# Performance work log

Measured on AMD Instinct MI355X. Metric: run time of the kernel, lower is better.

## Reference

```python
import jax, jax.numpy as jnp
import numpy as np

C = 256

def setup_inputs() -> dict:
    key = jax.random.key(0)
    ks = jax.random.split(key, 7)
    s = 1.0 / np.sqrt(C)
    x = jax.random.normal(ks[0], (4, C, 64, 64), dtype=jnp.float32)
    Wq = jax.random.uniform(ks[1], (C, C), jnp.float32, -s, s)
    bq = jax.random.uniform(ks[2], (C,), jnp.float32, -s, s)
    Wk = jax.random.uniform(ks[3], (C, C), jnp.float32, -s, s)
    bk = jax.random.uniform(ks[4], (C,), jnp.float32, -s, s)
    Wv = jax.random.uniform(ks[5], (C, C), jnp.float32, -s, s)
    bv = jax.random.uniform(ks[6], (C,), jnp.float32, -s, s)
    return {"x": x, "Wq": Wq, "bq": bq, "Wk": Wk, "bk": bk, "Wv": Wv, "bv": bv}

def reference(x, Wq, bq, Wk, bk, Wv, bv):
    B, Cc, H, W = x.shape
    N = H * W
    xf = x.reshape(B, Cc, N)                      # (B, C, N)
    # 1x1 conv == channel linear: out[b,o,n] = sum_c W[o,c] x[b,c,n] + b[o]
    q = jnp.einsum('oc,bcn->bno', Wq, xf) + bq    # (B, N, C)  proj_query^T
    k = jnp.einsum('oc,bcn->bon', Wk, xf) + bk[None, :, None]  # (B, C, N)
    v = jnp.einsum('oc,bcn->bon', Wv, xf) + bv[None, :, None]  # (B, C, N)
    energy = jnp.einsum('bnc,bcm->bnm', q, k)     # (B, N, N)
    attention = jax.nn.softmax(energy, axis=-1)
    # out = V @ attention^T : out[b,c,n] = sum_m v[b,c,m] * attention[b,n,m]
    out = jnp.einsum('bcm,bnm->bcn', v, attention)
    return out.reshape(B, Cc, H, W)
```

## Files before the change

kernel.cpp:

```cpp
#include <hip/hip_runtime.h>
#include <math.h>

#define BB 4
#define CC 256
#define NN 4096
#define KV 32

using half8 = __attribute__((ext_vector_type(8))) _Float16;
using f32x4 = __attribute__((ext_vector_type(4))) float;

__device__ __forceinline__ unsigned short f2h(float f) {
  _Float16 h = (_Float16)f;
  return __builtin_bit_cast(unsigned short, h);
}
__device__ __forceinline__ float h2f(unsigned short u) {
  return (float)__builtin_bit_cast(_Float16, u);
}

#define ASYNC16(g, l)                                                        \
  __builtin_amdgcn_global_load_lds(                                          \
      (const __attribute__((address_space(1))) unsigned int*)(g),            \
      (__attribute__((address_space(3))) unsigned int*)(l), 16, 0, 0)

__device__ __forceinline__ int row512_off(int r, int chunk) {
  return r * 256 + (((chunk & 24) | ((chunk ^ r) & 7)) << 3);
}
__device__ __forceinline__ int tile32_off(int r, int q) {
  return (r >> 1) * 64 + (((((r & 1) << 2) | q) ^ ((r >> 1) & 7)) & 7) * 8;
}
__device__ __forceinline__ int vt_off(int r, int chunk) {
  return r * 64 + (((chunk ^ r) & 7) << 3);
}

__global__ __launch_bounds__(256) void k_wcast(const float* __restrict__ Wq,
    const float* __restrict__ Wk, const float* __restrict__ Wv,
    unsigned short* __restrict__ Wt) {
  int id = blockIdx.x * 256 + threadIdx.x;
  int pos8 = id & 7, o = (id >> 3) & 255, ks = (id >> 11) & 3, p3 = id >> 13;
  const float* W = p3 == 0 ? Wq : (p3 == 1 ? Wk : Wv);
  int c = ks * 64 + ((pos8 ^ o) & 7) * 8;
  const float* src = W + (size_t)o * CC + c;
  float4 a = *(const float4*)(src);
  float4 b4 = *(const float4*)(src + 4);
  union { unsigned short u[8]; uint4 v4; } pk;
  pk.u[0] = f2h(a.x);  pk.u[1] = f2h(a.y);  pk.u[2] = f2h(a.z);  pk.u[3] = f2h(a.w);
  pk.u[4] = f2h(b4.x); pk.u[5] = f2h(b4.y); pk.u[6] = f2h(b4.z); pk.u[7] = f2h(b4.w);
  *(uint4*)(Wt + (size_t)id * 8) = pk.v4;
}

__global__ __launch_bounds__(512) void k_proj(const float* __restrict__ x,
    const unsigned short* __restrict__ Wt,
    const float* __restrict__ bq, const float* __restrict__ bk,
    const float* __restrict__ bv,
    unsigned short* __restrict__ Q, unsigned short* __restrict__ K,
    unsigned short* __restrict__ V) {
  __shared__ __align__(16) char ps[110848];
  float* xf = (float*)ps;
  unsigned short* xa = (unsigned short*)(ps + 8448);
  unsigned short* wh = (unsigned short*)(ps + 12544);
  int b = blockIdx.y, n0 = blockIdx.x * 32;
  int t = threadIdx.x, w = t >> 6, lane = t & 63, l15 = lane & 15, quad = lane >> 4;

  f32x4 z = {0.f, 0.f, 0.f, 0.f};
  f32x4 acc[3][2][2];
#pragma unroll
  for (int p3 = 0; p3 < 3; ++p3)
#pragma unroll
    for (int ct = 0; ct < 2; ++ct)
#pragma unroll
      for (int mt = 0; mt < 2; ++mt) acc[p3][ct][mt] = z;

  for (int ks = 0; ks < 4; ++ks) {
    if (ks) __syncthreads();
#pragma unroll
    for (int p3 = 0; p3 < 3; ++p3) {
      const char* wb = (const char*)(Wt + (size_t)(p3 * 4 + ks) * 16384);
#pragma unroll
      for (int p = 0; p < 4; ++p) {
        int c = p * 512 + t;
        ASYNC16(wb + c * 16, &wh[p3 * 16384 + (p * 512 + (w << 6)) * 8]);
      }
    }
    {
      int c = t >> 3, nl = (t & 7) * 4;
      float4 v = *(const float4*)(x + ((size_t)b * CC + ks * 64 + c) * NN + n0 + nl);
      float* d = xf + c * 33 + nl;
      d[0] = v.x; d[1] = v.y; d[2] = v.z; d[3] = v.w;
    }
    __syncthreads();
    {
      int n = t >> 4, cb = (t & 15) * 4;
      union { unsigned short u[4]; ushort4 v4; } tmp;
#pragma unroll
      for (int i = 0; i < 4; ++i) tmp.u[i] = f2h(xf[(cb + i) * 33 + n]);
      int ch = cb >> 3;
      *(ushort4*)&xa[n * 64 + (((ch ^ n) & 7) << 3) + (cb & 7)] = tmp.v4;
    }
    __syncthreads();
#pragma unroll
    for (int kc = 0; kc < 2; ++kc) {
      half8 af[2];
#pragma unroll
      for (int mt = 0; mt < 2; ++mt)
        af[mt] = *(const half8*)&xa[vt_off(mt * 16 + l15, kc * 4 + quad)];
#pragma unroll
      for (int p3 = 0; p3 < 3; ++p3)
#pragma unroll
        for (int ct = 0; ct < 2; ++ct) {
          half8 bf = *(const half8*)&wh[p3 * 16384 + vt_off(w * 32 + ct * 16 + l15, kc * 4 + quad)];
#pragma unroll
          for (int mt = 0; mt < 2; ++mt)
            acc[p3][ct][mt] = __builtin_amdgcn_mfma_f32_16x16x32_f16(af[mt], bf, acc[p3][ct][mt], 0, 0, 0);
        }
    }
  }
#pragma unroll
  for (int p3 = 0; p3 < 3; ++p3) {
    const float* bias = p3 == 0 ? bq : (p3 == 1 ? bk : bv);
#pragma unroll
    for (int ct = 0; ct < 2; ++ct) {
      float bv_ = bias[w * 32 + ct * 16 + l15];
#pragma unroll
      for (int mt = 0; mt < 2; ++mt)
#pragma unroll
        for (int r = 0; r < 4; ++r) acc[p3][ct][mt][r] += bv_;
    }
  }
#pragma unroll
  for (int p3 = 0; p3 < 2; ++p3) {
    __syncthreads();
    unsigned short* qo = (unsigned short*)ps;
#pragma unroll
    for (int ct = 0; ct < 2; ++ct)
#pragma unroll
      for (int mt = 0; mt < 2; ++mt)
#pragma unroll
        for (int r = 0; r < 4; ++r)
          qo[(mt * 16 + quad * 4 + r) * 264 + w * 32 + ct * 16 + l15] = f2h(acc[p3][ct][mt][r]);
    __syncthreads();
    unsigned short* outp = (p3 == 0 ? Q : K) + ((size_t)b * NN + n0) * CC;
#pragma unroll
    for (int p = 0; p < 2; ++p) {
      int f = p * 8192 + t * 16;
      int n = f >> 9, off = f & 511;
      *(uint4*)((char*)outp + (size_t)n * 512 + off) =
        *(const uint4*)((const char*)&qo[n * 264] + off);
    }
  }
  {
    __syncthreads();
    unsigned short* vo = (unsigned short*)ps;
#pragma unroll
    for (int ct = 0; ct < 2; ++ct)
#pragma unroll
      for (int mt = 0; mt < 2; ++mt)
#pragma unroll
        for (int r = 0; r < 4; ++r)
          vo[(w * 32 + ct * 16 + l15) * 36 + mt * 16 + quad * 4 + r] = f2h(acc[2][ct][mt][r]);
    __syncthreads();
#pragma unroll
    for (int p = 0; p < 2; ++p) {
      int id = p * 512 + t;
      int o = id >> 2, off = (id & 3) * 16;
      *(uint4*)((char*)(V + ((size_t)b * CC + o) * NN + n0) + off) =
        *(const uint4*)((const char*)&vo[o * 36] + off);
    }
  }
}

__global__ __launch_bounds__(512) void k_flash(const unsigned short* __restrict__ Q,
    const unsigned short* __restrict__ K, const unsigned short* __restrict__ V,
    float* __restrict__ out, unsigned short* __restrict__ opart,
    float* __restrict__ ml, int n_splits) {
  __shared__ __align__(16) char sm[83456];
  unsigned short* kt0 = (unsigned short*)sm;
  unsigned short* kt1 = (unsigned short*)(sm + 16384);
  unsigned short* vt0 = (unsigned short*)(sm + 32768);
  unsigned short* vt1 = (unsigned short*)(sm + 49152);
  unsigned short* pt0 = (unsigned short*)(sm + 65536);
  unsigned short* pt1 = (unsigned short*)(sm + 73728);
  float* al0 = (float*)(sm + 81920);
  float* al1 = (float*)(sm + 82432);
  float* ll  = (float*)(sm + 82944);
  int b = blockIdx.y, q0 = blockIdx.x * 128, split = blockIdx.z;
  int nt = (NN / KV) / n_splits;
  int t = threadIdx.x, w = t >> 6, lane = t & 63, l15 = lane & 15, quad = lane >> 4;
  int g = w >> 1, h = w & 1;

  half8 qf[8];
  const unsigned short* qrow = Q + ((size_t)b * NN + q0 + w * 16 + l15) * CC;
#pragma unroll
  for (int k = 0; k < 8; ++k) qf[k] = *(const half8*)(qrow + k * 32 + quad * 8);

  f32x4 z = {0.f, 0.f, 0.f, 0.f};
  f32x4 o_acc[2][8];
#pragma unroll
  for (int mt = 0; mt < 2; ++mt)
#pragma unroll
    for (int i = 0; i < 8; ++i) o_acc[mt][i] = z;
  float m_i[4], lp_[4];
#pragma unroll
  for (int r = 0; r < 4; ++r) { m_i[r] = -INFINITY; lp_[r] = 0.f; }

  int it_beg = split * nt, it_end = it_beg + nt;

  auto dma_k = [&](int it, unsigned short* dst) {
    const char* kb = (const char*)(K + ((size_t)b * NN + it * KV) * CC);
#pragma unroll
    for (int p = 0; p < 2; ++p) {
      int c = p * 512 + t;
      int r = c >> 5, lo = c & 31;
      int ch = (lo & 24) | ((lo ^ r) & 7);
      ASYNC16(kb + r * 512 + ch * 16, &dst[(p * 512 + (w << 6)) * 8]);
    }
  };
  auto dma_v = [&](int it, unsigned short* dst) {
    const char* vb = (const char*)(V + (size_t)b * CC * NN + it * KV);
#pragma unroll
    for (int p = 0; p < 2; ++p) {
      int id = p * 512 + t;
      int unit = id >> 3, u = id & 7;
      int x2 = u ^ (unit & 7);
      int r = unit * 2 + (x2 >> 2), ch = x2 & 3;
      ASYNC16(vb + (size_t)r * (NN * 2) + ch * 16, &dst[(p * 512 + (w << 6)) * 8]);
    }
  };

  auto pv_step = [&](const unsigned short* pprev, const unsigned short* vprev,
                     const float* alp) {
    f32x4 aa[2];
    aa[0] = *(const f32x4*)&alp[g * 32 + quad * 4];
    aa[1] = *(const f32x4*)&alp[g * 32 + 16 + quad * 4];
    int need = 0;
#pragma unroll
    for (int mt = 0; mt < 2; ++mt)
#pragma unroll
      for (int r = 0; r < 4; ++r) need |= (aa[mt][r] != 1.f);
    if (__any(need)) {
#pragma unroll
      for (int mt = 0; mt < 2; ++mt)
#pragma unroll
        for (int ct = 0; ct < 8; ++ct)
#pragma unroll
          for (int r = 0; r < 4; ++r) o_acc[mt][ct][r] *= aa[mt][r];
    }
    half8 af[2];
#pragma unroll
    for (int mt = 0; mt < 2; ++mt)
      af[mt] = *(const half8*)&pprev[tile32_off(g * 32 + mt * 16 + l15, quad)];
    __builtin_amdgcn_s_setprio(1);
#pragma unroll
    for (int ct = 0; ct < 8; ++ct) {
      half8 bf = *(const half8*)&vprev[tile32_off(h * 128 + ct * 16 + l15, quad)];
#pragma unroll
      for (int mt = 0; mt < 2; ++mt)
        o_acc[mt][ct] = __builtin_amdgcn_mfma_f32_16x16x32_f16(af[mt], bf, o_acc[mt][ct], 0, 0, 0);
    }
    __builtin_amdgcn_s_setprio(0);
  };

  dma_k(it_beg, (it_beg & 1) ? kt1 : kt0);

  for (int it = it_beg; it < it_end; ++it) {
    int par = it & 1;
    const unsigned short* kcur = par ? kt1 : kt0;
    unsigned short* knxt       = par ? kt0 : kt1;
    unsigned short* vcur       = par ? vt1 : vt0;
    const unsigned short* vprev = par ? vt0 : vt1;
    unsigned short* pcur       = par ? pt1 : pt0;
    const unsigned short* pprev = par ? pt0 : pt1;
    float* alc       = par ? al1 : al0;
    const float* alp = par ? al0 : al1;

    __syncthreads();

    if (it + 1 < it_end) dma_k(it + 1, knxt);
    dma_v(it, vcur);

    f32x4 sa[2];
    sa[0] = z; sa[1] = z;
    __builtin_amdgcn_s_setprio(1);
#pragma unroll
    for (int kk = 0; kk < 8; ++kk)
#pragma unroll
      for (int j = 0; j < 2; ++j) {
        half8 bf = *(const half8*)&kcur[row512_off(j * 16 + l15, kk * 4 + quad)];
        sa[j] = __builtin_amdgcn_mfma_f32_16x16x32_f16(qf[kk], bf, sa[j], 0, 0, 0);
      }
    __builtin_amdgcn_s_setprio(0);

    float mt4[4];
#pragma unroll
    for (int r = 0; r < 4; ++r) mt4[r] = fmaxf(sa[0][r], sa[1][r]);
#pragma unroll
    for (int off = 1; off < 16; off <<= 1)
#pragma unroll
      for (int r = 0; r < 4; ++r)
        mt4[r] = fmaxf(mt4[r], __shfl_xor(mt4[r], off, 64));
    float alpha[4];
#pragma unroll
    for (int r = 0; r < 4; ++r) {
      float mn = fmaxf(m_i[r], mt4[r]);
      alpha[r] = __expf(m_i[r] - mn);
      m_i[r] = mn;
    }
#pragma unroll
    for (int r = 0; r < 4; ++r) {
      float ls = 0.f;
#pragma unroll
      for (int j = 0; j < 2; ++j) {
        float p = __expf(sa[j][r] - m_i[r]);
        sa[j][r] = p;
        ls += p;
      }
      lp_[r] = lp_[r] * alpha[r] + ls;
    }
    if (l15 == 0) {
      f32x4 a4 = {alpha[0], alpha[1], alpha[2], alpha[3]};
      *(f32x4*)&alc[w * 16 + quad * 4] = a4;
    }
#pragma unroll
    for (int j = 0; j < 2; ++j)
#pragma unroll
      for (int r = 0; r < 4; ++r) {
        int row = w * 16 + quad * 4 + r;
        int ch = 2 * j + (l15 >> 3);
        pcur[tile32_off(row, ch) + (l15 & 7)] = f2h(sa[j][r]);
      }

    if (it > it_beg) pv_step(pprev, vprev, alp);
  }

  {
    int par = (it_end - 1) & 1;
    __syncthreads();
    pv_step(par ? pt1 : pt0, par ? vt1 : vt0, par ? al1 : al0);
  }

#pragma unroll
  for (int off = 1; off < 16; off <<= 1)
#pragma unroll
    for (int r = 0; r < 4; ++r)
      lp_[r] += __shfl_xor(lp_[r], off, 64);
  if (l15 == 0) {
#pragma unroll
    for (int r = 0; r < 4; ++r) ll[w * 16 + quad * 4 + r] = lp_[r];
  }
  if (n_splits != 1 && l15 == 0) {
    size_t qi = (size_t)q0 + w * 16 + quad * 4;
    float* mp = ml + ((size_t)(split * 2 + 0) * BB + b) * NN + qi;
    float* lq = ml + ((size_t)(split * 2 + 1) * BB + b) * NN + qi;
#pragma unroll
    for (int r = 0; r < 4; ++r) { mp[r] = m_i[r]; lq[r] = lp_[r]; }
  }
  __syncthreads();
  float sc[2][4];
#pragma unroll
  for (int mt = 0; mt < 2; ++mt)
#pragma unroll
    for (int r = 0; r < 4; ++r) {
      float lv = ll[g * 32 + mt * 16 + quad * 4 + r];
      sc[mt][r] = (n_splits == 1) ? 1.f / lv : 1.f;
    }

  float* od = (float*)sm;
  float* obf = out + (size_t)b * CC * NN + q0;
  unsigned short* obh = opart + ((size_t)split * BB + b) * CC * NN + q0;
#pragma unroll
  for (int pp = 0; pp < 8; ++pp) {
    __syncthreads();
    if (h == (pp >> 2)) {
#pragma unroll
      for (int cp = 0; cp < 2; ++cp) {
        int ct = (pp & 3) * 2 + cp;
#pragma unroll
        for (int mt = 0; mt < 2; ++mt)
#pragma unroll
          for (int r = 0; r < 4; ++r)
            od[(cp * 16 + l15) * 132 + g * 32 + mt * 16 + quad * 4 + r] =
                o_acc[mt][ct][r] * sc[mt][r];
      }
    }
    __syncthreads();
    if (n_splits == 1) {
#pragma unroll
      for (int p2 = 0; p2 < 2; ++p2) {
        int row = p2 * 16 + (t >> 5);
        *(float4*)(obf + (size_t)(pp * 32 + row) * NN + (t & 31) * 4) =
          *(const float4*)&od[row * 132 + (t & 31) * 4];
      }
    } else {
      int row = t >> 4, q8 = (t & 15) * 8;
      union { unsigned short u[8]; uint4 v4; } tmp;
#pragma unroll
      for (int i2 = 0; i2 < 8; ++i2) tmp.u[i2] = f2h(od[row * 132 + q8 + i2]);
      *(uint4*)(obh + (size_t)(pp * 32 + row) * NN + q8) = tmp.v4;
    }
  }
}

__global__ __launch_bounds__(256) void k_merge(const unsigned short* __restrict__ opart,
    const float* __restrict__ ml, float* __restrict__ out) {
  size_t i = ((size_t)blockIdx.x * 256 + threadIdx.x) * 4;
  int n = (int)(i & (NN - 1));
  int b = (int)(i >> 20);
  float4 m1 = *(const float4*)(ml + ((size_t)(0 * BB) + b) * NN + n);
  float4 l1 = *(const float4*)(ml + ((size_t)(1 * BB) + b) * NN + n);
  float4 m2 = *(const float4*)(ml + ((size_t)(2 * BB) + b) * NN + n);
  float4 l2 = *(const float4*)(ml + ((size_t)(3 * BB) + b) * NN + n);
  ushort4 o1 = *(const ushort4*)(opart + i);
  ushort4 o2 = *(const ushort4*)(opart + (size_t)BB * CC * NN + i);
  float4 res;
#define MRG(f, comp) { \
    float M = fmaxf(m1.f, m2.f); \
    float e1 = __expf(m1.f - M), e2 = __expf(m2.f - M); \
    res.f = (e1 * h2f(o1.comp) + e2 * h2f(o2.comp)) / (e1 * l1.f + e2 * l2.f); }
  MRG(x, x) MRG(y, y) MRG(z, z) MRG(w, w)
#undef MRG
  *(float4*)(out + i) = res;
}

extern "C" void kernel_launch(void* const* d_in, const int* in_sizes, int n_in,
                              void* d_out, int out_size, void* d_ws, size_t ws_size,
                              hipStream_t stream) {
  const float* x  = (const float*)d_in[0];
  const float* Wq = (const float*)d_in[1];
  const float* bq = (const float*)d_in[2];
  const float* Wk = (const float*)d_in[3];
  const float* bk = (const float*)d_in[4];
  const float* Wv = (const float*)d_in[5];
  const float* bv = (const float*)d_in[6];
  float* out = (float*)d_out;
  char* ws = (char*)d_ws;
  const size_t MB = 1024 * 1024;
  unsigned short* Qb = (unsigned short*)(ws);
  unsigned short* Kb = (unsigned short*)(ws + 8 * MB);
  unsigned short* Vb = (unsigned short*)(ws + 16 * MB);
  unsigned short* Op = (unsigned short*)(ws + 24 * MB);
  float*          Ml = (float*)(ws + 40 * MB);

  int ns = (ws_size >= 41 * MB) ? 2 : 1;
  unsigned short* Wt = (unsigned short*)(ns == 2 ? ws + 40 * MB + 256 * 1024
                                                 : ws + 24 * MB);

  k_wcast<<<dim3(96), 256, 0, stream>>>(Wq, Wk, Wv, Wt);
  k_proj<<<dim3(128, 4), 512, 0, stream>>>(x, Wt, bq, bk, bv, Qb, Kb, Vb);

  k_flash<<<dim3(32, 4, ns), 512, 0, stream>>>(Qb, Kb, Vb, out, Op, Ml, ns);
  if (ns == 2) k_merge<<<dim3(4096), 256, 0, stream>>>(Op, Ml, out);
}
```

Baseline: 234.0 us.

## Restructure flash attention kernel around 32x32 MFMA with 64-key tiles and split-K waves

The flash kernel now uses 32x32x16 MFMA with 64-key tiles, where each wave pair splits the key tile and the per-row max is exchanged through LDS. P is kept in registers and shuffled into the B operand instead of being written to LDS. The change also drops the separate alpha buffers, adds explicit waitcnt/barrier pipelining of the K/V DMA, and sums the two partial O accumulators in the epilogue. The goal is fewer LDS round trips and barriers per key and better MFMA efficiency, at the cost of larger LDS use (about 131KB) and heavier register pressure under launch_bounds(512,2).

New measurement: 240.4 us. 2.7% more time.

```diff
diff --git a/kernel.cpp b/kernel.cpp
--- a/kernel.cpp
+++ b/kernel.cpp
@@ -4,10 +4,11 @@
 #define BB 4
 #define CC 256
 #define NN 4096
-#define KV 32
+#define KV 64
 
 using half8 = __attribute__((ext_vector_type(8))) _Float16;
 using f32x4 = __attribute__((ext_vector_type(4))) float;
+using f32x16 = __attribute__((ext_vector_type(16))) float;
 
 __device__ __forceinline__ unsigned short f2h(float f) {
   _Float16 h = (_Float16)f;
@@ -22,12 +23,6 @@
       (const __attribute__((address_space(1))) unsigned int*)(g),            \
       (__attribute__((address_space(3))) unsigned int*)(l), 16, 0, 0)
 
-__device__ __forceinline__ int row512_off(int r, int chunk) {
-  return r * 256 + (((chunk & 24) | ((chunk ^ r) & 7)) << 3);
-}
-__device__ __forceinline__ int tile32_off(int r, int q) {
-  return (r >> 1) * 64 + (((((r & 1) << 2) | q) ^ ((r >> 1) & 7)) & 7) * 8;
-}
 __device__ __forceinline__ int vt_off(int r, int chunk) {
   return r * 64 + (((chunk ^ r) & 7) << 3);
 }
@@ -168,234 +163,231 @@
   }
 }
 
-__global__ __launch_bounds__(512) void k_flash(const unsigned short* __restrict__ Q,
+__global__ __launch_bounds__(512, 2) void k_flash(const unsigned short* __restrict__ Q,
     const unsigned short* __restrict__ K, const unsigned short* __restrict__ V,
     float* __restrict__ out, unsigned short* __restrict__ opart,
     float* __restrict__ ml, int n_splits) {
-  __shared__ __align__(16) char sm[83456];
+  __shared__ __align__(16) char sm[134144];
   unsigned short* kt0 = (unsigned short*)sm;
-  unsigned short* kt1 = (unsigned short*)(sm + 16384);
-  unsigned short* vt0 = (unsigned short*)(sm + 32768);
-  unsigned short* vt1 = (unsigned short*)(sm + 49152);
-  unsigned short* pt0 = (unsigned short*)(sm + 65536);
-  unsigned short* pt1 = (unsigned short*)(sm + 73728);
-  float* al0 = (float*)(sm + 81920);
-  float* al1 = (float*)(sm + 82432);
-  float* ll  = (float*)(sm + 82944);
+  unsigned short* kt1 = (unsigned short*)(sm + 32768);
+  unsigned short* vt0 = (unsigned short*)(sm + 65536);
+  unsigned short* vt1 = (unsigned short*)(sm + 98304);
+  float* mx  = (float*)(sm + 131072);
+  float* ll_ = (float*)(sm + 133120);
+
   int b = blockIdx.y, q0 = blockIdx.x * 128, split = blockIdx.z;
   int nt = (NN / KV) / n_splits;
-  int t = threadIdx.x, w = t >> 6, lane = t & 63, l15 = lane & 15, quad = lane >> 4;
-  int g = w >> 1, h = w & 1;
-
-  half8 qf[8];
-  const unsigned short* qrow = Q + ((size_t)b * NN + q0 + w * 16 + l15) * CC;
-#pragma unroll
-  for (int k = 0; k < 8; ++k) qf[k] = *(const half8*)(qrow + k * 32 + quad * 8);
-
-  f32x4 z = {0.f, 0.f, 0.f, 0.f};
-  f32x4 o_acc[2][8];
-#pragma unroll
-  for (int mt = 0; mt < 2; ++mt)
-#pragma unroll
-    for (int i = 0; i < 8; ++i) o_acc[mt][i] = z;
-  float m_i[4], lp_[4];
-#pragma unroll
-  for (int r = 0; r < 4; ++r) { m_i[r] = -INFINITY; lp_[r] = 0.f; }
+  int t = threadIdx.x, w = t >> 6, lane = t & 63;
+  int qn = lane & 31, hi = lane >> 5;
+  int qg = w >> 1, kth = w & 1;
+
+  half8 qf[16];
+  {
+    const unsigned short* qrow = Q + ((size_t)b * NN + q0 + qg * 32 + qn) * CC;
+#pragma unroll
+    for (int cs = 0; cs < 16; ++cs)
+      qf[cs] = *(const half8*)(qrow + cs * 16 + hi * 8);
+  }
+
+  f32x16 o_acc[8];
+#pragma unroll
+  for (int ct = 0; ct < 8; ++ct)
+#pragma unroll
+    for (int r = 0; r < 16; ++r) o_acc[ct][r] = 0.f;
+
+  f32x16 sa;
+  float m_i = -INFINITY, lp = 0.f, pm_carry = -INFINITY;
 
   int it_beg = split * nt, it_end = it_beg + nt;
 
   auto dma_k = [&](int it, unsigned short* dst) {
     const char* kb = (const char*)(K + ((size_t)b * NN + it * KV) * CC);
 #pragma unroll
-    for (int p = 0; p < 2; ++p) {
+    for (int p = 0; p < 4; ++p) {
       int c = p * 512 + t;
-      int r = c >> 5, lo = c & 31;
-      int ch = (lo & 24) | ((lo ^ r) & 7);
-      ASYNC16(kb + r * 512 + ch * 16, &dst[(p * 512 + (w << 6)) * 8]);
+      int r = c >> 5, chp = c & 31;
+      ASYNC16(kb + r * 512 + ((chp ^ (r & 31)) << 4), &dst[(p * 512 + (w << 6)) * 8]);
     }
   };
   auto dma_v = [&](int it, unsigned short* dst) {
-    const char* vb = (const char*)(V + (size_t)b * CC * NN + it * KV);
-#pragma unroll
-    for (int p = 0; p < 2; ++p) {
-      int id = p * 512 + t;
-      int unit = id >> 3, u = id & 7;
-      int x2 = u ^ (unit & 7);
-      int r = unit * 2 + (x2 >> 2), ch = x2 & 3;
-      ASYNC16(vb + (size_t)r * (NN * 2) + ch * 16, &dst[(p * 512 + (w << 6)) * 8]);
-    }
-  };
-
-  auto pv_step = [&](const unsigned short* pprev, const unsigned short* vprev,
-                     const float* alp) {
-    f32x4 aa[2];
-    aa[0] = *(const f32x4*)&alp[g * 32 + quad * 4];
-    aa[1] = *(const f32x4*)&alp[g * 32 + 16 + quad * 4];
-    int need = 0;
-#pragma unroll
-    for (int mt = 0; mt < 2; ++mt)
-#pragma unroll
-      for (int r = 0; r < 4; ++r) need |= (aa[mt][r] != 1.f);
-    if (__any(need)) {
-#pragma unroll
-      for (int mt = 0; mt < 2; ++mt)
-#pragma unroll
-        for (int ct = 0; ct < 8; ++ct)
-#pragma unroll
-          for (int r = 0; r < 4; ++r) o_acc[mt][ct][r] *= aa[mt][r];
-    }
-    half8 af[2];
-#pragma unroll
-    for (int mt = 0; mt < 2; ++mt)
-      af[mt] = *(const half8*)&pprev[tile32_off(g * 32 + mt * 16 + l15, quad)];
+    const char* vb = (const char*)(V + (size_t)b * CC * NN) + it * 128;
+#pragma unroll
+    for (int p = 0; p < 4; ++p) {
+      int c = p * 512 + t;
+      int r = c >> 3, chp = c & 7;
+      ASYNC16(vb + (size_t)r * 8192 + ((chp ^ (r & 7)) << 4), &dst[(p * 512 + (w << 6)) * 8]);
+    }
+  };
+
+  auto qkt = [&](const unsigned short* kc) {
+#pragma unroll
+    for (int r = 0; r < 16; ++r) sa[r] = 0.f;
     __builtin_amdgcn_s_setprio(1);
 #pragma unroll
-    for (int ct = 0; ct < 8; ++ct) {
-      half8 bf = *(const half8*)&vprev[tile32_off(h * 128 + ct * 16 + l15, quad)];
-#pragma unroll
-      for (int mt = 0; mt < 2; ++mt)
-        o_acc[mt][ct] = __builtin_amdgcn_mfma_f32_16x16x32_f16(af[mt], bf, o_acc[mt][ct], 0, 0, 0);
+    for (int cs = 0; cs < 16; ++cs) {
+      half8 kf = *(const half8*)&kc[(kth * 32 + qn) * 256 + ((((cs * 2 + hi) ^ qn) & 31) << 3)];
+      sa = __builtin_amdgcn_mfma_f32_32x32x16_f16(kf, qf[cs], sa, 0, 0, 0);
     }
     __builtin_amdgcn_s_setprio(0);
   };
 
+  auto partial_max = [&](int par) {
+    float pm = sa[0];
+#pragma unroll
+    for (int r = 1; r < 16; ++r) pm = fmaxf(pm, sa[r]);
+    pm = fmaxf(pm, __shfl_xor(pm, 32, 64));
+    pm_carry = pm;
+    if (lane < 32) mx[(par * 2 + kth) * 128 + qg * 32 + lane] = pm;
+  };
+
+  unsigned int g0x, g0y, g1x, g1y, g2x, g2y, g3x, g3y;
+
+  auto finish_sm = [&](int prevpar) {
+    float prt = mx[(prevpar * 2 + (kth ^ 1)) * 128 + qg * 32 + qn];
+    float mtile = fmaxf(pm_carry, prt);
+    float mnew = fmaxf(m_i, mtile);
+    float alpha = __expf(m_i - mnew);
+    m_i = mnew;
+    float ls = 0.f;
+#pragma unroll
+    for (int r = 0; r < 16; ++r) {
+      float p = __expf(sa[r] - mnew);
+      sa[r] = p;
+      ls += p;
+    }
+    ls += __shfl_xor(ls, 32, 64);
+    lp = lp * alpha + ls;
+    g0x = (unsigned)f2h(sa[0])  | ((unsigned)f2h(sa[1])  << 16);
+    g0y = (unsigned)f2h(sa[2])  | ((unsigned)f2h(sa[3])  << 16);
+    g1x = (unsigned)f2h(sa[4])  | ((unsigned)f2h(sa[5])  << 16);
+    g1y = (unsigned)f2h(sa[6])  | ((unsigned)f2h(sa[7])  << 16);
+    g2x = (unsigned)f2h(sa[8])  | ((unsigned)f2h(sa[9])  << 16);
+    g2y = (unsigned)f2h(sa[10]) | ((unsigned)f2h(sa[11]) << 16);
+    g3x = (unsigned)f2h(sa[12]) | ((unsigned)f2h(sa[13]) << 16);
+    g3y = (unsigned)f2h(sa[14]) | ((unsigned)f2h(sa[15]) << 16);
+    if (!__all(alpha == 1.0f)) {
+#pragma unroll
+      for (int ct = 0; ct < 8; ++ct)
+#pragma unroll
+        for (int r = 0; r < 16; ++r) o_acc[ct][r] *= alpha;
+    }
+  };
+
+  auto pv = [&](const unsigned short* vp) {
+    __builtin_amdgcn_s_setprio(1);
+#pragma unroll
+    for (int s = 0; s < 2; ++s) {
+      unsigned int ax = s ? g2x : g0x, ay = s ? g2y : g0y;
+      unsigned int bx = s ? g3x : g1x, by = s ? g3y : g1y;
+      unsigned int vx = hi ? ax : bx, vy = hi ? ay : by;
+      unsigned int xx = (unsigned int)__shfl_xor((int)vx, 32, 64);
+      unsigned int xy = (unsigned int)__shfl_xor((int)vy, 32, 64);
+      union { unsigned int u[4]; half8 h; } bf;
+      bf.u[0] = hi ? xx : ax;
+      bf.u[1] = hi ? xy : ay;
+      bf.u[2] = hi ? bx : xx;
+      bf.u[3] = hi ? by : xy;
+#pragma unroll
+      for (int ct = 0; ct < 8; ++ct) {
+        half8 af = *(const half8*)&vp[(ct * 32 + qn) * 64 + ((((kth * 4 + s * 2 + hi) ^ (qn & 7)) & 7) << 3)];
+        o_acc[ct] = __builtin_amdgcn_mfma_f32_32x32x16_f16(af, bf.h, o_acc[ct], 0, 0, 0);
+      }
+    }
+    __builtin_amdgcn_s_setprio(0);
+  };
+
   dma_k(it_beg, (it_beg & 1) ? kt1 : kt0);
-
-  for (int it = it_beg; it < it_end; ++it) {
+  dma_v(it_beg, (it_beg & 1) ? vt1 : vt0);
+  asm volatile("s_waitcnt vmcnt(4) lgkmcnt(0)" ::: "memory");
+  __builtin_amdgcn_s_barrier();
+  __builtin_amdgcn_sched_barrier(0);
+  {
+    int par = it_beg & 1;
+    if (it_beg + 1 < it_end) {
+      dma_k(it_beg + 1, par ? kt0 : kt1);
+      dma_v(it_beg + 1, par ? vt0 : vt1);
+    }
+    qkt(par ? kt1 : kt0);
+    partial_max(par);
+  }
+  for (int it = it_beg + 1; it < it_end; ++it) {
     int par = it & 1;
     const unsigned short* kcur = par ? kt1 : kt0;
-    unsigned short* knxt       = par ? kt0 : kt1;
-    unsigned short* vcur       = par ? vt1 : vt0;
-    const unsigned short* vprev = par ? vt0 : vt1;
-    unsigned short* pcur       = par ? pt1 : pt0;
-    const unsigned short* pprev = par ? pt0 : pt1;
-    float* alc       = par ? al1 : al0;
-    const float* alp = par ? al0 : al1;
-
-    __syncthreads();
-
+    unsigned short* knxt = par ? kt0 : kt1;
+    unsigned short* vprv = par ? vt0 : vt1;
+    asm volatile("s_waitcnt vmcnt(4) lgkmcnt(0)" ::: "memory");
+    __builtin_amdgcn_s_barrier();
+    __builtin_amdgcn_sched_barrier(0);
     if (it + 1 < it_end) dma_k(it + 1, knxt);
-    dma_v(it, vcur);
-
-    f32x4 sa[2];
-    sa[0] = z; sa[1] = z;
-    __builtin_amdgcn_s_setprio(1);
-#pragma unroll
-    for (int kk = 0; kk < 8; ++kk)
-#pragma unroll
-      for (int j = 0; j < 2; ++j) {
-        half8 bf = *(const half8*)&kcur[row512_off(j * 16 + l15, kk * 4 + quad)];
-        sa[j] = __builtin_amdgcn_mfma_f32_16x16x32_f16(qf[kk], bf, sa[j], 0, 0, 0);
-      }
-    __builtin_amdgcn_s_setprio(0);
-
-    float mt4[4];
-#pragma unroll
-    for (int r = 0; r < 4; ++r) mt4[r] = fmaxf(sa[0][r], sa[1][r]);
-#pragma unroll
-    for (int off = 1; off < 16; off <<= 1)
-#pragma unroll
-      for (int r = 0; r < 4; ++r)
-        mt4[r] = fmaxf(mt4[r], __shfl_xor(mt4[r], off, 64));
-    float alpha[4];
-#pragma unroll
-    for (int r = 0; r < 4; ++r) {
-      float mn = fmaxf(m_i[r], mt4[r]);
-      alpha[r] = __expf(m_i[r] - mn);
-      m_i[r] = mn;
-    }
-#pragma unroll
-    for (int r = 0; r < 4; ++r) {
-      float ls = 0.f;
-#pragma unroll
-      for (int j = 0; j < 2; ++j) {
-        float p = __expf(sa[j][r] - m_i[r]);
-        sa[j][r] = p;
-        ls += p;
-      }
-      lp_[r] = lp_[r] * alpha[r] + ls;
-    }
-    if (l15 == 0) {
-      f32x4 a4 = {alpha[0], alpha[1], alpha[2], alpha[3]};
-      *(f32x4*)&alc[w * 16 + quad * 4] = a4;
-    }
-#pragma unroll
-    for (int j = 0; j < 2; ++j)
-#pragma unroll
-      for (int r = 0; r < 4; ++r) {
-        int row = w * 16 + quad * 4 + r;
-        int ch = 2 * j + (l15 >> 3);
-        pcur[tile32_off(row, ch) + (l15 & 7)] = f2h(sa[j][r]);
-      }
-
-    if (it > it_beg) pv_step(pprev, vprev, alp);
-  }
-
+    finish_sm(par ^ 1);
+    pv(vprv);
+    __builtin_amdgcn_sched_barrier(0);
+    __builtin_amdgcn_s_barrier();
+    __builtin_amdgcn_sched_barrier(0);
+    if (it + 1 < it_end) dma_v(it + 1, vprv);
+    qkt(kcur);
+    partial_max(par);
+  }
+  __syncthreads();
   {
     int par = (it_end - 1) & 1;
-    __syncthreads();
-    pv_step(par ? pt1 : pt0, par ? vt1 : vt0, par ? al1 : al0);
-  }
-
-#pragma unroll
-  for (int off = 1; off < 16; off <<= 1)
-#pragma unroll
-    for (int r = 0; r < 4; ++r)
-      lp_[r] += __shfl_xor(lp_[r], off, 64);
-  if (l15 == 0) {
-#pragma unroll
-    for (int r = 0; r < 4; ++r) ll[w * 16 + quad * 4 + r] = lp_[r];
-  }
-  if (n_splits != 1 && l15 == 0) {
-    size_t qi = (size_t)q0 + w * 16 + quad * 4;
-    float* mp = ml + ((size_t)(split * 2 + 0) * BB + b) * NN + qi;
-    float* lq = ml + ((size_t)(split * 2 + 1) * BB + b) * NN + qi;
-#pragma unroll
-    for (int r = 0; r < 4; ++r) { mp[r] = m_i[r]; lq[r] = lp_[r]; }
-  }
+    finish_sm(par);
+    pv(par ? vt1 : vt0);
+  }
+
+  if (lane < 32) ll_[kth * 128 + qg * 32 + lane] = lp;
   __syncthreads();
-  float sc[2][4];
-#pragma unroll
-  for (int mt = 0; mt < 2; ++mt)
-#pragma unroll
-    for (int r = 0; r < 4; ++r) {
-      float lv = ll[g * 32 + mt * 16 + quad * 4 + r];
-      sc[mt][r] = (n_splits == 1) ? 1.f / lv : 1.f;
-    }
-
-  float* od = (float*)sm;
+  float* od0 = (float*)sm;
+  float* od1 = od0 + 32 * 132;
+  float* linv = (float*)(sm + 33792);
+  if (t < 128) {
+    float l = ll_[t] + ll_[128 + t];
+    linv[t] = (n_splits == 1) ? 1.0f / l : 1.0f;
+  }
+  if (n_splits != 1 && kth == 0 && lane < 32) {
+    size_t qi = (size_t)q0 + qg * 32 + lane;
+    float lt = ll_[qg * 32 + lane] + ll_[128 + qg * 32 + lane];
+    ml[((size_t)(split * 2 + 0) * BB + b) * NN + qi] = m_i;
+    ml[((size_t)(split * 2 + 1) * BB + b) * NN + qi] = lt;
+  }
+  __syncthreads();
+
   float* obf = out + (size_t)b * CC * NN + q0;
   unsigned short* obh = opart + ((size_t)split * BB + b) * CC * NN + q0;
 #pragma unroll
-  for (int pp = 0; pp < 8; ++pp) {
-    __syncthreads();
-    if (h == (pp >> 2)) {
-#pragma unroll
-      for (int cp = 0; cp < 2; ++cp) {
-        int ct = (pp & 3) * 2 + cp;
-#pragma unroll
-        for (int mt = 0; mt < 2; ++mt)
-#pragma unroll
-          for (int r = 0; r < 4; ++r)
-            od[(cp * 16 + l15) * 132 + g * 32 + mt * 16 + quad * 4 + r] =
-                o_acc[mt][ct][r] * sc[mt][r];
+  for (int ct = 0; ct < 8; ++ct) {
+    float* od = kth ? od1 : od0;
+#pragma unroll
+    for (int r = 0; r < 16; ++r) {
+      int cl = (r & 3) + 8 * (r >> 2) + 4 * hi;
+      od[cl * 132 + qg * 32 + qn] = o_acc[ct][r];
+    }
+    __syncthreads();
+    {
+      int row = t >> 4, q8 = (t & 15) * 8;
+      f32x4 a0 = *(const f32x4*)&od0[row * 132 + q8];
+      f32x4 a1 = *(const f32x4*)&od0[row * 132 + q8 + 4];
+      f32x4 b0 = *(const f32x4*)&od1[row * 132 + q8];
+      f32x4 b1 = *(const f32x4*)&od1[row * 132 + q8 + 4];
+      f32x4 l0 = *(const f32x4*)&linv[q8];
+      f32x4 l1 = *(const f32x4*)&linv[q8 + 4];
+      f32x4 s0, s1;
+#pragma unroll
+      for (int i = 0; i < 4; ++i) {
+        s0[i] = (a0[i] + b0[i]) * l0[i];
+        s1[i] = (a1[i] + b1[i]) * l1[i];
       }
-    }
-    __syncthreads();
-    if (n_splits == 1) {
-#pragma unroll
-      for (int p2 = 0; p2 < 2; ++p2) {
-        int row = p2 * 16 + (t >> 5);
-        *(float4*)(obf + (size_t)(pp * 32 + row) * NN + (t & 31) * 4) =
-          *(const float4*)&od[row * 132 + (t & 31) * 4];
+      if (n_splits == 1) {
+        *(f32x4*)(obf + (size_t)(ct * 32 + row) * NN + q8) = s0;
+        *(f32x4*)(obf + (size_t)(ct * 32 + row) * NN + q8 + 4) = s1;
+      } else {
+        union { unsigned short u[8]; uint4 v4; } tmp;
+#pragma unroll
+        for (int i = 0; i < 4; ++i) { tmp.u[i] = f2h(s0[i]); tmp.u[4 + i] = f2h(s1[i]); }
+        *(uint4*)(obh + (size_t)(ct * 32 + row) * NN + q8) = tmp.v4;
       }
-    } else {
-      int row = t >> 4, q8 = (t & 15) * 8;
-      union { unsigned short u[8]; uint4 v4; } tmp;
-#pragma unroll
-      for (int i2 = 0; i2 < 8; ++i2) tmp.u[i2] = f2h(od[row * 132 + q8 + i2]);
-      *(uint4*)(obh + (size_t)(pp * 32 + row) * NN + q8) = tmp.v4;
-    }
+    }
+    __syncthreads();
   }
 }
 
```
